# Optimization experiments

Measured on AMD Instinct MI355X. Metric: run time of the kernel, lower is better.

Reference implementation:

```python
import jax, jax.numpy as jnp
import numpy as np

EMBED_DIM = 768
NUM_HEADS = 12
HEAD_DIM = EMBED_DIM // NUM_HEADS


def setup_inputs() -> dict:
    key = jax.random.key(0)
    k1, k2, k3, k4, k5 = jax.random.split(key, 5)
    B, S, D = 2, 4096, EMBED_DIM
    scale = 1.0 / np.sqrt(D)
    return {
        "x": jax.random.normal(k1, (B, S, D), dtype=jnp.float32),
        "Wqkv": jax.random.normal(k2, (D, 3 * D), dtype=jnp.float32) * scale,
        "bqkv": jax.random.normal(k3, (3 * D,), dtype=jnp.float32) * 0.02,
        "Wout": jax.random.normal(k4, (D, D), dtype=jnp.float32) * scale,
        "bout": jax.random.normal(k5, (D,), dtype=jnp.float32) * 0.02,
    }


def reference(x, Wqkv, bqkv, Wout, bout):
    B, S, D = x.shape
    H, Hd = NUM_HEADS, HEAD_DIM
    # fused QKV projection: [B,S,3D]
    qkv = x @ Wqkv + bqkv
    q, k, v = jnp.split(qkv, 3, axis=-1)
    # [B,S,D] -> [B,H,S,Hd]
    q = q.reshape(B, S, H, Hd).transpose(0, 2, 1, 3)
    k = k.reshape(B, S, H, Hd).transpose(0, 2, 1, 3)
    v = v.reshape(B, S, H, Hd).transpose(0, 2, 1, 3)
    # causal SDPA (dropout_p = 0)
    scores = jnp.einsum("bhsd,bhtd->bhst", q, k) / jnp.sqrt(jnp.asarray(Hd, x.dtype))
    causal = jnp.tril(jnp.ones((S, S), dtype=bool))  # [S,S]
    scores = jnp.where(causal[None, None], scores, jnp.finfo(x.dtype).min)
    attn = jax.nn.softmax(scores, axis=-1)
    y = jnp.einsum("bhst,bhtd->bhsd", attn, v)  # [B,H,S,Hd]
    y = y.transpose(0, 2, 1, 3).reshape(B, S, D)
    return y @ Wout + bout
```

## Files before the change

### kernel.cpp

```cpp
#include <hip/hip_runtime.h>

#define S_LEN 4096
#define NH 12
#define HD 64
#define DMODEL 768
#define BATCH 2
#define MTOT (BATCH * S_LEN)

typedef __bf16 bf16x8 __attribute__((ext_vector_type(8)));
typedef __bf16 bf16x4 __attribute__((ext_vector_type(4)));
typedef float f32x4 __attribute__((ext_vector_type(4)));
typedef float f32x8 __attribute__((ext_vector_type(8)));

#define SM_SCALE_LOG2E 0.18033688f
#define SLAB_STRIDE 8448

__device__ __forceinline__ f32x4 f32x4_zero() {
  f32x4 z = {0.f, 0.f, 0.f, 0.f};
  return z;
}

__device__ __forceinline__ void async16(const __bf16* g, void* l) {
  __builtin_amdgcn_global_load_lds(
      (const __attribute__((address_space(1))) void*)g,
      (__attribute__((address_space(3))) void*)l, 16, 0, 0);
}

__global__ __launch_bounds__(256) void cvt_f32_bf16(const float* __restrict__ in,
                                                    __bf16* __restrict__ out, int n8) {
  int i = blockIdx.x * 256 + threadIdx.x;
  if (i >= n8) return;
  f32x8 a = ((const f32x8*)in)[i];
  bf16x8 o;
#pragma unroll
  for (int j = 0; j < 8; ++j) o[j] = (__bf16)a[j];
  ((bf16x8*)out)[i] = o;
}

__global__ __launch_bounds__(256) void transpose_cvt(const float* __restrict__ in,
                                                     __bf16* __restrict__ out, int N) {
  __shared__ __bf16 t[64][72];
  int kb = blockIdx.x * 64, nb = blockIdx.y * 64;
  int c = threadIdx.x & 63, r0 = threadIdx.x >> 6;
#pragma unroll
  for (int i = 0; i < 16; ++i) {
    int r = r0 * 16 + i;
    t[c][r] = (__bf16)in[(size_t)(kb + r) * N + nb + c];
  }
  __syncthreads();
#pragma unroll
  for (int i = 0; i < 16; ++i) {
    int r = r0 * 16 + i;
    out[(size_t)(nb + r) * DMODEL + kb + c] = t[r][c];
  }
}

__device__ __forceinline__ void gemm128_bt(const __bf16* __restrict__ A,
                                           const __bf16* __restrict__ Bt,
                                           int m0, int n0, int K,
                                           __bf16* Alds, __bf16* Blds,
                                           f32x4 acc[4][4]) {
  const int tid = threadIdx.x;
  const int l = tid & 63, w = tid >> 6;
  const int wr = w >> 1, wc = w & 1;
  const int g = l >> 4, ln = l & 15;

  const int rr = tid >> 3;
  const int sx = (tid & 7) ^ (rr & 7);
  const __bf16* As = A + (size_t)(m0 + rr) * K + sx * 8;
  const __bf16* Bs = Bt + (size_t)(n0 + rr) * K + sx * 8;
  char* Ad = (char*)Alds + (w << 10);
  char* Bd = (char*)Blds + (w << 10);

  for (int k0 = 0; k0 < K; k0 += 64) {
#pragma unroll
    for (int i = 0; i < 4; ++i) {
      async16(As + (size_t)(i * 32) * K + k0, Ad + i * 4096);
      async16(Bs + (size_t)(i * 32) * K + k0, Bd + i * 4096);
    }
    __syncthreads();
#pragma unroll
    for (int kk = 0; kk < 2; ++kk) {
      bf16x8 af[4], bfr[4];
#pragma unroll
      for (int mi = 0; mi < 4; ++mi) {
        int row = wr * 64 + mi * 16 + ln;
        af[mi] = *(const bf16x8*)(Alds + row * 64 + ((((kk << 2) + g) ^ (row & 7)) << 3));
      }
#pragma unroll
      for (int ni = 0; ni < 4; ++ni) {
        int row = wc * 64 + ni * 16 + ln;
        bfr[ni] = *(const bf16x8*)(Blds + row * 64 + ((((kk << 2) + g) ^ (row & 7)) << 3));
      }
#pragma unroll
      for (int mi = 0; mi < 4; ++mi)
#pragma unroll
        for (int ni = 0; ni < 4; ++ni)
          acc[mi][ni] =
              __builtin_amdgcn_mfma_f32_16x16x32_bf16(af[mi], bfr[ni], acc[mi][ni], 0, 0, 0);
    }
    __syncthreads();
  }
}

__global__ __launch_bounds__(256) void gemm_qkv(const __bf16* __restrict__ xb,
                                                const __bf16* __restrict__ Wt,
                                                const float* __restrict__ bqkv,
                                                __bf16* __restrict__ Qo,
                                                __bf16* __restrict__ Ko,
                                                __bf16* __restrict__ Vto) {
  __shared__ __bf16 Alds[128 * 64];
  __shared__ __bf16 Blds[128 * 64];
  int bm = blockIdx.x & 63, bn = blockIdx.x >> 6;
  int m0 = bm * 128, n0 = bn * 128;
  f32x4 acc[4][4];
#pragma unroll
  for (int i = 0; i < 4; ++i)
#pragma unroll
    for (int j = 0; j < 4; ++j) acc[i][j] = f32x4_zero();
  gemm128_bt(xb, Wt, m0, n0, DMODEL, Alds, Blds, acc);

  const int l = threadIdx.x & 63, w = threadIdx.x >> 6;
  const int wr = w >> 1, wc = w & 1, g = l >> 4, ln = l & 15;
#pragma unroll
  for (int ni = 0; ni < 4; ++ni) {
    int ncol = n0 + wc * 64 + ni * 16 + ln;
    int which = ncol / DMODEL;
    int dd = ncol - which * DMODEL;
    int h = dd >> 6, hd = dd & 63;
    float bias = bqkv[ncol];
    if (which == 2) {
#pragma unroll
      for (int mi = 0; mi < 4; ++mi)
#pragma unroll
        for (int r = 0; r < 4; ++r) {
          int mrow = m0 + wr * 64 + mi * 16 + 4 * g + r;
          int b = mrow >> 12, s = mrow & (S_LEN - 1);
          float v = acc[mi][ni][r] + bias;
          Vto[(((size_t)(b * NH + h) * HD) + hd) * S_LEN + s] = (__bf16)v;
        }
    } else {
      __bf16* op = (which == 0) ? Qo : Ko;
      const float scl = (which == 0) ? SM_SCALE_LOG2E : 1.0f;
#pragma unroll
      for (int mi = 0; mi < 4; ++mi)
#pragma unroll
        for (int r = 0; r < 4; ++r) {
          int mrow = m0 + wr * 64 + mi * 16 + 4 * g + r;
          int b = mrow >> 12, s = mrow & (S_LEN - 1);
          float v = (acc[mi][ni][r] + bias) * scl;
          op[((((size_t)b * NH + h) * S_LEN) + s) * HD + hd] = (__bf16)v;
        }
    }
  }
}

__global__ __launch_bounds__(256) void gemm_out(const __bf16* __restrict__ yb,
                                                const __bf16* __restrict__ Wt,
                                                const float* __restrict__ bout,
                                                float* __restrict__ out) {
  __shared__ __bf16 Alds[128 * 64];
  __shared__ __bf16 Blds[128 * 64];
  int bm = blockIdx.x & 63, bn = blockIdx.x >> 6;
  int m0 = bm * 128, n0 = bn * 128;
  f32x4 acc[4][4];
#pragma unroll
  for (int i = 0; i < 4; ++i)
#pragma unroll
    for (int j = 0; j < 4; ++j) acc[i][j] = f32x4_zero();
  gemm128_bt(yb, Wt, m0, n0, DMODEL, Alds, Blds, acc);

  const int l = threadIdx.x & 63, w = threadIdx.x >> 6;
  const int wr = w >> 1, wc = w & 1, g = l >> 4, ln = l & 15;
#pragma unroll
  for (int ni = 0; ni < 4; ++ni) {
    int ncol = n0 + wc * 64 + ni * 16 + ln;
    float bias = bout[ncol];
#pragma unroll
    for (int mi = 0; mi < 4; ++mi)
#pragma unroll
      for (int r = 0; r < 4; ++r) {
        int mrow = m0 + wr * 64 + mi * 16 + 4 * g + r;
        out[(size_t)mrow * DMODEL + ncol] = acc[mi][ni][r] + bias;
      }
  }
}

__global__ __launch_bounds__(256) void attn_fwd14(const __bf16* __restrict__ Q,
                                                  const __bf16* __restrict__ K,
                                                  const __bf16* __restrict__ Vt,
                                                  __bf16* __restrict__ Y,
                                                  char* __restrict__ Po) {
  __shared__ __bf16 KVl[2][2][4096];
  __shared__ char Plb[4][2048];

  const int tid = threadIdx.x;
  const int wv = tid >> 6, l = tid & 63;
  const int g = l >> 4, ln = l & 15;
  const int bi = blockIdx.x;
  const int xcd = bi & 7, j = bi >> 3;
  const int head = xcd * 3 + (j % 3);
  const int r_ = j / 3;

  int c, t0, t1, part;
  bool split;
  if (r_ < 64) {
    c = 63 - (r_ >> 1);
    part = r_ & 1;
    int T = c + 1;
    int h = (T + 1) >> 1;
    t0 = part ? h : 0;
    t1 = part ? T : h;
    split = true;
  } else {
    c = 95 - r_;
    part = 0;
    t0 = 0;
    t1 = c + 1;
    split = false;
  }
  const int q0 = 64 * c + 16 * wv;
  const int thr = 16 * wv + ln;
  const bool hasDiag = (t1 == c + 1);

  const size_t hb = (size_t)head * (S_LEN * HD);
  const __bf16* Qh = Q + hb;
  const __bf16* Kh = K + hb;
  const __bf16* Vh = Vt + hb;

  const int sw = (ln & 7) << 4;
  char* Pw = Plb[wv] + ln * 128;

  const int r0 = tid >> 3;
  const int s0 = (tid & 7) ^ (r0 & 7);
  const size_t kL0 = (size_t)r0 * HD + s0 * 8;
  const size_t kL1 = kL0 + (size_t)32 * HD;
  const size_t vL0 = (size_t)r0 * S_LEN + s0 * 8;
  const size_t vL1 = vL0 + (size_t)32 * S_LEN;
  const int ldsoff = wv << 10;

  bf16x8 qf[2];
#pragma unroll
  for (int t = 0; t < 2; ++t)
    qf[t] = *(const bf16x8*)(Qh + (size_t)(q0 + ln) * HD + 32 * t + 8 * g);

  bf16x8 ones;
#pragma unroll
  for (int t = 0; t < 8; ++t) ones[t] = (__bf16)1.0f;

  f32x4 o[4], o5;
#pragma unroll
  for (int nt = 0; nt < 4; ++nt) o[nt] = f32x4_zero();
  o5 = f32x4_zero();

  const __bf16* kq = Kh + (size_t)t0 * 64 * HD;
  const __bf16* vq = Vh + t0 * 64;
  {
    char* Kd = (char*)&KVl[0][0][0] + ldsoff;
    char* Vd = (char*)&KVl[0][1][0] + ldsoff;
    async16(kq + kL0, Kd);
    async16(kq + kL1, Kd + 4096);
    async16(vq + vL0, Vd);
    async16(vq + vL1, Vd + 4096);
    __syncthreads();
  }
  kq += (size_t)64 * HD;
  vq += 64;

  int cur = 0;
  for (int i = t0; i < t1; ++i) {
    const bool more = (i + 1) < t1;
    if (more) {
      char* Kd = (char*)&KVl[cur ^ 1][0][0] + ldsoff;
      char* Vd = (char*)&KVl[cur ^ 1][1][0] + ldsoff;
      async16(kq + kL0, Kd);
      async16(kq + kL1, Kd + 4096);
      async16(vq + vL0, Vd);
      async16(vq + vL1, Vd + 4096);
      kq += (size_t)64 * HD;
      vq += 64;
    }

    const __bf16* Kl = &KVl[cur][0][0];
    const __bf16* Vl = &KVl[cur][1][0];
    const bool diag = hasDiag && (i == c);

    if (!diag) {
#pragma unroll
      for (int jt = 0; jt < 4; ++jt) {
        int row = 16 * jt + ln;
        bf16x8 kf0 = *(const bf16x8*)(Kl + row * 64 + ((g ^ (row & 7)) << 3));
        bf16x8 kf1 = *(const bf16x8*)(Kl + row * 64 + (((4 + g) ^ (row & 7)) << 3));
        f32x4 z = f32x4_zero();
        z = __builtin_amdgcn_mfma_f32_16x16x32_bf16(kf0, qf[0], z, 0, 0, 0);
        z = __builtin_amdgcn_mfma_f32_16x16x32_bf16(kf1, qf[1], z, 0, 0, 0);
        bf16x4 qd;
#pragma unroll
        for (int r = 0; r < 4; ++r) qd[r] = (__bf16)__builtin_exp2f(z[r]);
        *(bf16x4*)(Pw + ((32 * jt + 8 * g) ^ sw)) = qd;
      }
    } else {
#pragma unroll
      for (int jt = 0; jt < 4; ++jt) {
        int row = 16 * jt + ln;
        bf16x8 kf0 = *(const bf16x8*)(Kl + row * 64 + ((g ^ (row & 7)) << 3));
        bf16x8 kf1 = *(const bf16x8*)(Kl + row * 64 + (((4 + g) ^ (row & 7)) << 3));
        f32x4 z = f32x4_zero();
        z = __builtin_amdgcn_mfma_f32_16x16x32_bf16(kf0, qf[0], z, 0, 0, 0);
        z = __builtin_amdgcn_mfma_f32_16x16x32_bf16(kf1, qf[1], z, 0, 0, 0);
        bf16x4 qd;
#pragma unroll
        for (int r = 0; r < 4; ++r) {
          float pv = __builtin_exp2f(z[r]);
          if (16 * jt + 4 * g + r > thr) pv = 0.f;
          qd[r] = (__bf16)pv;
        }
        *(bf16x4*)(Pw + ((32 * jt + 8 * g) ^ sw)) = qd;
      }
    }

    bf16x8 pa0 = *(const bf16x8*)(Pw + ((16 * g) ^ sw));
    bf16x8 pa1 = *(const bf16x8*)(Pw + ((64 + 16 * g) ^ sw));
    __builtin_amdgcn_s_setprio(1);
    o5 = __builtin_amdgcn_mfma_f32_16x16x32_bf16(pa0, ones, o5, 0, 0, 0);
    o5 = __builtin_amdgcn_mfma_f32_16x16x32_bf16(pa1, ones, o5, 0, 0, 0);
#pragma unroll
    for (int nt = 0; nt < 4; ++nt) {
      int row = 16 * nt + ln;
      bf16x8 vf0 = *(const bf16x8*)(Vl + row * 64 + ((g ^ (row & 7)) << 3));
      bf16x8 vf1 = *(const bf16x8*)(Vl + row * 64 + (((4 + g) ^ (row & 7)) << 3));
      o[nt] = __builtin_amdgcn_mfma_f32_16x16x32_bf16(pa0, vf0, o[nt], 0, 0, 0);
      o[nt] = __builtin_amdgcn_mfma_f32_16x16x32_bf16(pa1, vf1, o[nt], 0, 0, 0);
    }
    __builtin_amdgcn_s_setprio(0);

    if (more) __syncthreads();
    cur ^= 1;
  }

  if (!split) {
    const int bb = head / NH, hh = head - bb * NH;
    __bf16* Yp = Y + ((size_t)bb * S_LEN) * DMODEL + hh * HD;
#pragma unroll
    for (int r = 0; r < 4; ++r) {
      float inv = 1.0f / o5[r];
      int qr = q0 + 4 * g + r;
#pragma unroll
      for (int nt = 0; nt < 4; ++nt)
        Yp[(size_t)qr * DMODEL + 16 * nt + ln] = (__bf16)(o[nt][r] * inv);
    }
  } else {
    char* slab = Po + (size_t)(((head << 5) + (c - 32)) * 2 + part) * SLAB_STRIDE;
#pragma unroll
    for (int r = 0; r < 4; ++r) {
      int rowL = 16 * wv + 4 * g + r;
#pragma unroll
      for (int nt = 0; nt < 4; ++nt)
        *(__bf16*)(slab + (rowL * 64 + 16 * nt + ln) * 2) = (__bf16)o[nt][r];
      if (ln == 0) *(float*)(slab + 8192 + rowL * 4) = o5[r];
    }
  }
}

__global__ __launch_bounds__(256) void attn_combine(const char* __restrict__ Po,
                                                    __bf16* __restrict__ Y) {
  const int blk = blockIdx.x;
  const int head = blk >> 6, rem = blk & 63;
  const int cc = rem >> 1, half = rem & 1;
  const int c = cc + 32;
  const char* s0 = Po + (size_t)(((head << 5) + cc) * 2) * SLAB_STRIDE;
  const char* s1 = s0 + SLAB_STRIDE;
  const int tid = threadIdx.x;
  const int row = half * 32 + (tid >> 3), d0 = (tid & 7) * 8;

  bf16x8 a = *(const bf16x8*)(s0 + (row * 64 + d0) * 2);
  bf16x8 b = *(const bf16x8*)(s1 + (row * 64 + d0) * 2);
  float rs = *(const float*)(s0 + 8192 + row * 4) + *(const float*)(s1 + 8192 + row * 4);
  float inv = 1.0f / rs;

  const int bb = head / NH, hh = head - bb * NH;
  __bf16* yp = Y + ((size_t)bb * S_LEN + 64 * c + row) * DMODEL + hh * HD + d0;
  bf16x8 o;
#pragma unroll
  for (int j = 0; j < 8; ++j) o[j] = (__bf16)(((float)a[j] + (float)b[j]) * inv);
  *(bf16x8*)yp = o;
}

extern "C" void kernel_launch(void* const* d_in, const int* in_sizes, int n_in,
                              void* d_out, int out_size, void* d_ws, size_t ws_size,
                              hipStream_t stream) {
  const float* x = (const float*)d_in[0];
  const float* Wqkv = (const float*)d_in[1];
  const float* bqkv = (const float*)d_in[2];
  const float* Wout = (const float*)d_in[3];
  const float* bout = (const float*)d_in[4];
  float* out = (float*)d_out;

  char* ws = (char*)d_ws;
  size_t off = 0;
  auto take = [&](size_t bytes) {
    char* p = ws + off;
    off += bytes;
    return p;
  };
  const size_t MD2 = (size_t)MTOT * DMODEL * 2;
  __bf16* xb = (__bf16*)take(MD2);
  __bf16* Wqkv_t = (__bf16*)take((size_t)3 * DMODEL * DMODEL * 2);
  __bf16* Wout_t = (__bf16*)take((size_t)DMODEL * DMODEL * 2);
  __bf16* Qb = (__bf16*)take(MD2);
  __bf16* Kb = (__bf16*)take(MD2);
  __bf16* Vtb = (__bf16*)take(MD2);
  __bf16* Yb = (__bf16*)take(MD2);
  char* Po = take((size_t)1536 * SLAB_STRIDE);

  int n8 = MTOT * DMODEL / 8;
  cvt_f32_bf16<<<(n8 + 255) / 256, 256, 0, stream>>>(x, xb, n8);
  transpose_cvt<<<dim3(DMODEL / 64, 3 * DMODEL / 64), 256, 0, stream>>>(Wqkv, Wqkv_t, 3 * DMODEL);
  transpose_cvt<<<dim3(DMODEL / 64, DMODEL / 64), 256, 0, stream>>>(Wout, Wout_t, DMODEL);
  gemm_qkv<<<64 * (3 * DMODEL / 128), 256, 0, stream>>>(xb, Wqkv_t, bqkv, Qb, Kb, Vtb);
  attn_fwd14<<<2304, 256, 0, stream>>>(Qb, Kb, Vtb, Yb, Po);
  attn_combine<<<1536, 256, 0, stream>>>(Po, Yb);
  gemm_out<<<64 * (DMODEL / 128), 256, 0, stream>>>(Yb, Wout_t, bout, out);
}
```

Before: 183.2 us.

## Process two 64-row query tiles per attention block to share K/V loads

The attention kernel now gives each block 128 query rows, split into two 64-row subtiles (A and B). Both subtiles are computed from the same double-buffered K/V tiles in shared memory, which halves K/V global traffic and the number of barriers per query row. The work split, slab layout and combine indexing are rescaled to match, and the launch drops to half as many blocks. In exchange each block holds more registers (two sets of accumulators and Q fragments), and coarser blocks may balance the causal workload less evenly.

New measurement: 212.9 us. +16.2%, slower.

```diff
diff --git a/kernel.cpp b/kernel.cpp
--- a/kernel.cpp
+++ b/kernel.cpp
@@ -13,7 +13,7 @@
 typedef float f32x8 __attribute__((ext_vector_type(8)));
 
 #define SM_SCALE_LOG2E 0.18033688f
-#define SLAB_STRIDE 8448
+#define SLAB_STRIDE 16896
 
 __device__ __forceinline__ f32x4 f32x4_zero() {
   f32x4 z = {0.f, 0.f, 0.f, 0.f};
@@ -186,7 +186,7 @@
   }
 }
 
-__global__ __launch_bounds__(256) void attn_fwd14(const __bf16* __restrict__ Q,
+__global__ __launch_bounds__(256) void attn_fwd16(const __bf16* __restrict__ Q,
                                                   const __bf16* __restrict__ K,
                                                   const __bf16* __restrict__ Vt,
                                                   __bf16* __restrict__ Y,
@@ -204,24 +204,24 @@
 
   int c, t0, t1, part;
   bool split;
-  if (r_ < 64) {
-    c = 63 - (r_ >> 1);
+  if (r_ < 32) {
+    c = 31 - (r_ >> 1);
     part = r_ & 1;
-    int T = c + 1;
-    int h = (T + 1) >> 1;
+    int h = c + 1;
     t0 = part ? h : 0;
-    t1 = part ? T : h;
+    t1 = part ? 2 * c + 2 : h;
     split = true;
   } else {
-    c = 95 - r_;
+    c = 47 - r_;
     part = 0;
     t0 = 0;
-    t1 = c + 1;
+    t1 = 2 * c + 2;
     split = false;
   }
-  const int q0 = 64 * c + 16 * wv;
+  const int q0A = 128 * c + 16 * wv;
+  const int q0B = q0A + 64;
   const int thr = 16 * wv + ln;
-  const bool hasDiag = (t1 == c + 1);
+  const int iA = 2 * c, iB = 2 * c + 1;
 
   const size_t hb = (size_t)head * (S_LEN * HD);
   const __bf16* Qh = Q + hb;
@@ -239,19 +239,25 @@
   const size_t vL1 = vL0 + (size_t)32 * S_LEN;
   const int ldsoff = wv << 10;
 
-  bf16x8 qf[2];
-#pragma unroll
-  for (int t = 0; t < 2; ++t)
-    qf[t] = *(const bf16x8*)(Qh + (size_t)(q0 + ln) * HD + 32 * t + 8 * g);
+  bf16x8 qfA[2], qfB[2];
+#pragma unroll
+  for (int t = 0; t < 2; ++t) {
+    qfA[t] = *(const bf16x8*)(Qh + (size_t)(q0A + ln) * HD + 32 * t + 8 * g);
+    qfB[t] = *(const bf16x8*)(Qh + (size_t)(q0B + ln) * HD + 32 * t + 8 * g);
+  }
 
   bf16x8 ones;
 #pragma unroll
   for (int t = 0; t < 8; ++t) ones[t] = (__bf16)1.0f;
 
-  f32x4 o[4], o5;
-#pragma unroll
-  for (int nt = 0; nt < 4; ++nt) o[nt] = f32x4_zero();
-  o5 = f32x4_zero();
+  f32x4 oA[4], oB[4], o5A, o5B;
+#pragma unroll
+  for (int nt = 0; nt < 4; ++nt) {
+    oA[nt] = f32x4_zero();
+    oB[nt] = f32x4_zero();
+  }
+  o5A = f32x4_zero();
+  o5B = f32x4_zero();
 
   const __bf16* kq = Kh + (size_t)t0 * 64 * HD;
   const __bf16* vq = Vh + t0 * 64;
@@ -283,56 +289,108 @@
 
     const __bf16* Kl = &KVl[cur][0][0];
     const __bf16* Vl = &KVl[cur][1][0];
-    const bool diag = hasDiag && (i == c);
-
-    if (!diag) {
-#pragma unroll
-      for (int jt = 0; jt < 4; ++jt) {
-        int row = 16 * jt + ln;
-        bf16x8 kf0 = *(const bf16x8*)(Kl + row * 64 + ((g ^ (row & 7)) << 3));
-        bf16x8 kf1 = *(const bf16x8*)(Kl + row * 64 + (((4 + g) ^ (row & 7)) << 3));
-        f32x4 z = f32x4_zero();
-        z = __builtin_amdgcn_mfma_f32_16x16x32_bf16(kf0, qf[0], z, 0, 0, 0);
-        z = __builtin_amdgcn_mfma_f32_16x16x32_bf16(kf1, qf[1], z, 0, 0, 0);
-        bf16x4 qd;
-#pragma unroll
-        for (int r = 0; r < 4; ++r) qd[r] = (__bf16)__builtin_exp2f(z[r]);
-        *(bf16x4*)(Pw + ((32 * jt + 8 * g) ^ sw)) = qd;
-      }
-    } else {
-#pragma unroll
-      for (int jt = 0; jt < 4; ++jt) {
-        int row = 16 * jt + ln;
-        bf16x8 kf0 = *(const bf16x8*)(Kl + row * 64 + ((g ^ (row & 7)) << 3));
-        bf16x8 kf1 = *(const bf16x8*)(Kl + row * 64 + (((4 + g) ^ (row & 7)) << 3));
-        f32x4 z = f32x4_zero();
-        z = __builtin_amdgcn_mfma_f32_16x16x32_bf16(kf0, qf[0], z, 0, 0, 0);
-        z = __builtin_amdgcn_mfma_f32_16x16x32_bf16(kf1, qf[1], z, 0, 0, 0);
-        bf16x4 qd;
-#pragma unroll
-        for (int r = 0; r < 4; ++r) {
-          float pv = __builtin_exp2f(z[r]);
-          if (16 * jt + 4 * g + r > thr) pv = 0.f;
-          qd[r] = (__bf16)pv;
-        }
-        *(bf16x4*)(Pw + ((32 * jt + 8 * g) ^ sw)) = qd;
-      }
-    }
-
-    bf16x8 pa0 = *(const bf16x8*)(Pw + ((16 * g) ^ sw));
-    bf16x8 pa1 = *(const bf16x8*)(Pw + ((64 + 16 * g) ^ sw));
-    __builtin_amdgcn_s_setprio(1);
-    o5 = __builtin_amdgcn_mfma_f32_16x16x32_bf16(pa0, ones, o5, 0, 0, 0);
-    o5 = __builtin_amdgcn_mfma_f32_16x16x32_bf16(pa1, ones, o5, 0, 0, 0);
-#pragma unroll
-    for (int nt = 0; nt < 4; ++nt) {
-      int row = 16 * nt + ln;
-      bf16x8 vf0 = *(const bf16x8*)(Vl + row * 64 + ((g ^ (row & 7)) << 3));
-      bf16x8 vf1 = *(const bf16x8*)(Vl + row * 64 + (((4 + g) ^ (row & 7)) << 3));
-      o[nt] = __builtin_amdgcn_mfma_f32_16x16x32_bf16(pa0, vf0, o[nt], 0, 0, 0);
-      o[nt] = __builtin_amdgcn_mfma_f32_16x16x32_bf16(pa1, vf1, o[nt], 0, 0, 0);
-    }
-    __builtin_amdgcn_s_setprio(0);
+
+    if (i <= iA) {
+      const bool diag = (i == iA);
+      if (!diag) {
+#pragma unroll
+        for (int jt = 0; jt < 4; ++jt) {
+          int row = 16 * jt + ln;
+          bf16x8 kf0 = *(const bf16x8*)(Kl + row * 64 + ((g ^ (row & 7)) << 3));
+          bf16x8 kf1 = *(const bf16x8*)(Kl + row * 64 + (((4 + g) ^ (row & 7)) << 3));
+          f32x4 z = f32x4_zero();
+          z = __builtin_amdgcn_mfma_f32_16x16x32_bf16(kf0, qfA[0], z, 0, 0, 0);
+          z = __builtin_amdgcn_mfma_f32_16x16x32_bf16(kf1, qfA[1], z, 0, 0, 0);
+          bf16x4 qd;
+#pragma unroll
+          for (int r = 0; r < 4; ++r) qd[r] = (__bf16)__builtin_exp2f(z[r]);
+          *(bf16x4*)(Pw + ((32 * jt + 8 * g) ^ sw)) = qd;
+        }
+      } else {
+#pragma unroll
+        for (int jt = 0; jt < 4; ++jt) {
+          int row = 16 * jt + ln;
+          bf16x8 kf0 = *(const bf16x8*)(Kl + row * 64 + ((g ^ (row & 7)) << 3));
+          bf16x8 kf1 = *(const bf16x8*)(Kl + row * 64 + (((4 + g) ^ (row & 7)) << 3));
+          f32x4 z = f32x4_zero();
+          z = __builtin_amdgcn_mfma_f32_16x16x32_bf16(kf0, qfA[0], z, 0, 0, 0);
+          z = __builtin_amdgcn_mfma_f32_16x16x32_bf16(kf1, qfA[1], z, 0, 0, 0);
+          bf16x4 qd;
+#pragma unroll
+          for (int r = 0; r < 4; ++r) {
+            float pv = __builtin_exp2f(z[r]);
+            if (16 * jt + 4 * g + r > thr) pv = 0.f;
+            qd[r] = (__bf16)pv;
+          }
+          *(bf16x4*)(Pw + ((32 * jt + 8 * g) ^ sw)) = qd;
+        }
+      }
+      bf16x8 pa0 = *(const bf16x8*)(Pw + ((16 * g) ^ sw));
+      bf16x8 pa1 = *(const bf16x8*)(Pw + ((64 + 16 * g) ^ sw));
+      __builtin_amdgcn_s_setprio(1);
+      o5A = __builtin_amdgcn_mfma_f32_16x16x32_bf16(pa0, ones, o5A, 0, 0, 0);
+      o5A = __builtin_amdgcn_mfma_f32_16x16x32_bf16(pa1, ones, o5A, 0, 0, 0);
+#pragma unroll
+      for (int nt = 0; nt < 4; ++nt) {
+        int row = 16 * nt + ln;
+        bf16x8 vf0 = *(const bf16x8*)(Vl + row * 64 + ((g ^ (row & 7)) << 3));
+        bf16x8 vf1 = *(const bf16x8*)(Vl + row * 64 + (((4 + g) ^ (row & 7)) << 3));
+        oA[nt] = __builtin_amdgcn_mfma_f32_16x16x32_bf16(pa0, vf0, oA[nt], 0, 0, 0);
+        oA[nt] = __builtin_amdgcn_mfma_f32_16x16x32_bf16(pa1, vf1, oA[nt], 0, 0, 0);
+      }
+      __builtin_amdgcn_s_setprio(0);
+    }
+
+    {
+      const bool diag = (i == iB);
+      if (!diag) {
+#pragma unroll
+        for (int jt = 0; jt < 4; ++jt) {
+          int row = 16 * jt + ln;
+          bf16x8 kf0 = *(const bf16x8*)(Kl + row * 64 + ((g ^ (row & 7)) << 3));
+          bf16x8 kf1 = *(const bf16x8*)(Kl + row * 64 + (((4 + g) ^ (row & 7)) << 3));
+          f32x4 z = f32x4_zero();
+          z = __builtin_amdgcn_mfma_f32_16x16x32_bf16(kf0, qfB[0], z, 0, 0, 0);
+          z = __builtin_amdgcn_mfma_f32_16x16x32_bf16(kf1, qfB[1], z, 0, 0, 0);
+          bf16x4 qd;
+#pragma unroll
+          for (int r = 0; r < 4; ++r) qd[r] = (__bf16)__builtin_exp2f(z[r]);
+          *(bf16x4*)(Pw + ((32 * jt + 8 * g) ^ sw)) = qd;
+        }
+      } else {
+#pragma unroll
+        for (int jt = 0; jt < 4; ++jt) {
+          int row = 16 * jt + ln;
+          bf16x8 kf0 = *(const bf16x8*)(Kl + row * 64 + ((g ^ (row & 7)) << 3));
+          bf16x8 kf1 = *(const bf16x8*)(Kl + row * 64 + (((4 + g) ^ (row & 7)) << 3));
+          f32x4 z = f32x4_zero();
+          z = __builtin_amdgcn_mfma_f32_16x16x32_bf16(kf0, qfB[0], z, 0, 0, 0);
+          z = __builtin_amdgcn_mfma_f32_16x16x32_bf16(kf1, qfB[1], z, 0, 0, 0);
+          bf16x4 qd;
+#pragma unroll
+          for (int r = 0; r < 4; ++r) {
+            float pv = __builtin_exp2f(z[r]);
+            if (16 * jt + 4 * g + r > thr) pv = 0.f;
+            qd[r] = (__bf16)pv;
+          }
+          *(bf16x4*)(Pw + ((32 * jt + 8 * g) ^ sw)) = qd;
+        }
+      }
+      bf16x8 pa0 = *(const bf16x8*)(Pw + ((16 * g) ^ sw));
+      bf16x8 pa1 = *(const bf16x8*)(Pw + ((64 + 16 * g) ^ sw));
+      __builtin_amdgcn_s_setprio(1);
+      o5B = __builtin_amdgcn_mfma_f32_16x16x32_bf16(pa0, ones, o5B, 0, 0, 0);
+      o5B = __builtin_amdgcn_mfma_f32_16x16x32_bf16(pa1, ones, o5B, 0, 0, 0);
+#pragma unroll
+      for (int nt = 0; nt < 4; ++nt) {
+        int row = 16 * nt + ln;
+        bf16x8 vf0 = *(const bf16x8*)(Vl + row * 64 + ((g ^ (row & 7)) << 3));
+        bf16x8 vf1 = *(const bf16x8*)(Vl + row * 64 + (((4 + g) ^ (row & 7)) << 3));
+        oB[nt] = __builtin_amdgcn_mfma_f32_16x16x32_bf16(pa0, vf0, oB[nt], 0, 0, 0);
+        oB[nt] = __builtin_amdgcn_mfma_f32_16x16x32_bf16(pa1, vf1, oB[nt], 0, 0, 0);
+      }
+      __builtin_amdgcn_s_setprio(0);
+    }
 
     if (more) __syncthreads();
     cur ^= 1;
@@ -343,21 +401,29 @@
     __bf16* Yp = Y + ((size_t)bb * S_LEN) * DMODEL + hh * HD;
 #pragma unroll
     for (int r = 0; r < 4; ++r) {
-      float inv = 1.0f / o5[r];
-      int qr = q0 + 4 * g + r;
-#pragma unroll
-      for (int nt = 0; nt < 4; ++nt)
-        Yp[(size_t)qr * DMODEL + 16 * nt + ln] = (__bf16)(o[nt][r] * inv);
+      float invA = 1.0f / o5A[r];
+      float invB = 1.0f / o5B[r];
+      int qrA = q0A + 4 * g + r, qrB = q0B + 4 * g + r;
+#pragma unroll
+      for (int nt = 0; nt < 4; ++nt) {
+        Yp[(size_t)qrA * DMODEL + 16 * nt + ln] = (__bf16)(oA[nt][r] * invA);
+        Yp[(size_t)qrB * DMODEL + 16 * nt + ln] = (__bf16)(oB[nt][r] * invB);
+      }
     }
   } else {
-    char* slab = Po + (size_t)(((head << 5) + (c - 32)) * 2 + part) * SLAB_STRIDE;
+    char* slab = Po + (size_t)(((head << 4) + (c - 16)) * 2 + part) * SLAB_STRIDE;
 #pragma unroll
     for (int r = 0; r < 4; ++r) {
-      int rowL = 16 * wv + 4 * g + r;
-#pragma unroll
-      for (int nt = 0; nt < 4; ++nt)
-        *(__bf16*)(slab + (rowL * 64 + 16 * nt + ln) * 2) = (__bf16)o[nt][r];
-      if (ln == 0) *(float*)(slab + 8192 + rowL * 4) = o5[r];
+      int rowA = 16 * wv + 4 * g + r, rowB = 64 + rowA;
+#pragma unroll
+      for (int nt = 0; nt < 4; ++nt) {
+        *(__bf16*)(slab + (rowA * 64 + 16 * nt + ln) * 2) = (__bf16)oA[nt][r];
+        *(__bf16*)(slab + (rowB * 64 + 16 * nt + ln) * 2) = (__bf16)oB[nt][r];
+      }
+      if (ln == 0) {
+        *(float*)(slab + 16384 + rowA * 4) = o5A[r];
+        *(float*)(slab + 16384 + rowB * 4) = o5B[r];
+      }
     }
   }
 }
@@ -366,20 +432,20 @@
                                                     __bf16* __restrict__ Y) {
   const int blk = blockIdx.x;
   const int head = blk >> 6, rem = blk & 63;
-  const int cc = rem >> 1, half = rem & 1;
-  const int c = cc + 32;
-  const char* s0 = Po + (size_t)(((head << 5) + cc) * 2) * SLAB_STRIDE;
+  const int cc = rem >> 2, quarter = rem & 3;
+  const int c = cc + 16;
+  const char* s0 = Po + (size_t)(((head << 4) + cc) * 2) * SLAB_STRIDE;
   const char* s1 = s0 + SLAB_STRIDE;
   const int tid = threadIdx.x;
-  const int row = half * 32 + (tid >> 3), d0 = (tid & 7) * 8;
+  const int row = quarter * 32 + (tid >> 3), d0 = (tid & 7) * 8;
 
   bf16x8 a = *(const bf16x8*)(s0 + (row * 64 + d0) * 2);
   bf16x8 b = *(const bf16x8*)(s1 + (row * 64 + d0) * 2);
-  float rs = *(const float*)(s0 + 8192 + row * 4) + *(const float*)(s1 + 8192 + row * 4);
+  float rs = *(const float*)(s0 + 16384 + row * 4) + *(const float*)(s1 + 16384 + row * 4);
   float inv = 1.0f / rs;
 
   const int bb = head / NH, hh = head - bb * NH;
-  __bf16* yp = Y + ((size_t)bb * S_LEN + 64 * c + row) * DMODEL + hh * HD + d0;
+  __bf16* yp = Y + ((size_t)bb * S_LEN + 128 * c + row) * DMODEL + hh * HD + d0;
   bf16x8 o;
 #pragma unroll
   for (int j = 0; j < 8; ++j) o[j] = (__bf16)(((float)a[j] + (float)b[j]) * inv);
@@ -411,14 +477,14 @@
   __bf16* Kb = (__bf16*)take(MD2);
   __bf16* Vtb = (__bf16*)take(MD2);
   __bf16* Yb = (__bf16*)take(MD2);
-  char* Po = take((size_t)1536 * SLAB_STRIDE);
+  char* Po = take((size_t)768 * SLAB_STRIDE);
 
   int n8 = MTOT * DMODEL / 8;
   cvt_f32_bf16<<<(n8 + 255) / 256, 256, 0, stream>>>(x, xb, n8);
   transpose_cvt<<<dim3(DMODEL / 64, 3 * DMODEL / 64), 256, 0, stream>>>(Wqkv, Wqkv_t, 3 * DMODEL);
   transpose_cvt<<<dim3(DMODEL / 64, DMODEL / 64), 256, 0, stream>>>(Wout, Wout_t, DMODEL);
   gemm_qkv<<<64 * (3 * DMODEL / 128), 256, 0, stream>>>(xb, Wqkv_t, bqkv, Qb, Kb, Vtb);
-  attn_fwd14<<<2304, 256, 0, stream>>>(Qb, Kb, Vtb, Yb, Po);
+  attn_fwd16<<<1152, 256, 0, stream>>>(Qb, Kb, Vtb, Yb, Po);
   attn_combine<<<1536, 256, 0, stream>>>(Po, Yb);
   gemm_out<<<64 * (DMODEL / 128), 256, 0, stream>>>(Yb, Wout_t, bout, out);
 }
```

## Split causal attention KV range into up to four parts by query-block length

Applied to the files above, without the earlier changes.

Replaces the two-way KV split for the longest query blocks with a graded split: the longest 16 query blocks per head get four parts, the next 16 get three, the next 16 get two, and the shortest stay unsplit. Work per block becomes more uniform and the grid grows from 2304 to 3840 blocks, reducing the long tail of the causal attention kernel. The combine kernel now sums a variable number of partial slabs for more rows, adding more partial-output traffic and combine work.

Measured after the change: 179.1 us. -2.3%, faster.

```diff
diff --git a/kernel.cpp b/kernel.cpp
--- a/kernel.cpp
+++ b/kernel.cpp
@@ -186,7 +186,7 @@
   }
 }
 
-__global__ __launch_bounds__(256) void attn_fwd14(const __bf16* __restrict__ Q,
+__global__ __launch_bounds__(256) void attn_fwd17(const __bf16* __restrict__ Q,
                                                   const __bf16* __restrict__ K,
                                                   const __bf16* __restrict__ Vt,
                                                   __bf16* __restrict__ Y,
@@ -202,26 +202,39 @@
   const int head = xcd * 3 + (j % 3);
   const int r_ = j / 3;
 
-  int c, t0, t1, part;
+  int c, part, np;
   bool split;
   if (r_ < 64) {
-    c = 63 - (r_ >> 1);
-    part = r_ & 1;
-    int T = c + 1;
-    int h = (T + 1) >> 1;
-    t0 = part ? h : 0;
-    t1 = part ? T : h;
+    c = 63 - (r_ >> 2);
+    part = r_ & 3;
+    np = 4;
+    split = true;
+  } else if (r_ < 112) {
+    int q = r_ - 64;
+    c = 47 - q / 3;
+    part = q % 3;
+    np = 3;
+    split = true;
+  } else if (r_ < 144) {
+    int q = r_ - 112;
+    c = 31 - (q >> 1);
+    part = q & 1;
+    np = 2;
     split = true;
   } else {
-    c = 95 - r_;
+    c = 159 - r_;
     part = 0;
-    t0 = 0;
-    t1 = c + 1;
+    np = 1;
     split = false;
   }
+  const int T = c + 1;
+  const int base = T / np, rem = T % np;
+  const int t0 = part * base + (part < rem ? part : rem);
+  const int t1 = t0 + base + (part < rem ? 1 : 0);
+
   const int q0 = 64 * c + 16 * wv;
   const int thr = 16 * wv + ln;
-  const bool hasDiag = (t1 == c + 1);
+  const bool hasDiag = (t1 == T);
 
   const size_t hb = (size_t)head * (S_LEN * HD);
   const __bf16* Qh = Q + hb;
@@ -350,7 +363,11 @@
         Yp[(size_t)qr * DMODEL + 16 * nt + ln] = (__bf16)(o[nt][r] * inv);
     }
   } else {
-    char* slab = Po + (size_t)(((head << 5) + (c - 32)) * 2 + part) * SLAB_STRIDE;
+    int soff;
+    if (c < 32) soff = (c - 16) * 2 + part;
+    else if (c < 48) soff = 32 + (c - 32) * 3 + part;
+    else soff = 80 + (c - 48) * 4 + part;
+    char* slab = Po + ((size_t)head * 144 + soff) * SLAB_STRIDE;
 #pragma unroll
     for (int r = 0; r < 4; ++r) {
       int rowL = 16 * wv + 4 * g + r;
@@ -365,24 +382,39 @@
 __global__ __launch_bounds__(256) void attn_combine(const char* __restrict__ Po,
                                                     __bf16* __restrict__ Y) {
   const int blk = blockIdx.x;
-  const int head = blk >> 6, rem = blk & 63;
+  const int head = blk / 96, rem = blk - head * 96;
   const int cc = rem >> 1, half = rem & 1;
-  const int c = cc + 32;
-  const char* s0 = Po + (size_t)(((head << 5) + cc) * 2) * SLAB_STRIDE;
-  const char* s1 = s0 + SLAB_STRIDE;
+  const int c = cc + 16;
+  int np, boff;
+  if (c < 32) {
+    np = 2;
+    boff = (c - 16) * 2;
+  } else if (c < 48) {
+    np = 3;
+    boff = 32 + (c - 32) * 3;
+  } else {
+    np = 4;
+    boff = 80 + (c - 48) * 4;
+  }
+  const char* s = Po + ((size_t)head * 144 + boff) * SLAB_STRIDE;
   const int tid = threadIdx.x;
   const int row = half * 32 + (tid >> 3), d0 = (tid & 7) * 8;
 
-  bf16x8 a = *(const bf16x8*)(s0 + (row * 64 + d0) * 2);
-  bf16x8 b = *(const bf16x8*)(s1 + (row * 64 + d0) * 2);
-  float rs = *(const float*)(s0 + 8192 + row * 4) + *(const float*)(s1 + 8192 + row * 4);
+  float acc[8] = {0.f, 0.f, 0.f, 0.f, 0.f, 0.f, 0.f, 0.f};
+  float rs = 0.f;
+  for (int p = 0; p < np; ++p) {
+    bf16x8 a = *(const bf16x8*)(s + (size_t)p * SLAB_STRIDE + (row * 64 + d0) * 2);
+#pragma unroll
+    for (int j = 0; j < 8; ++j) acc[j] += (float)a[j];
+    rs += *(const float*)(s + (size_t)p * SLAB_STRIDE + 8192 + row * 4);
+  }
   float inv = 1.0f / rs;
 
   const int bb = head / NH, hh = head - bb * NH;
   __bf16* yp = Y + ((size_t)bb * S_LEN + 64 * c + row) * DMODEL + hh * HD + d0;
   bf16x8 o;
 #pragma unroll
-  for (int j = 0; j < 8; ++j) o[j] = (__bf16)(((float)a[j] + (float)b[j]) * inv);
+  for (int j = 0; j < 8; ++j) o[j] = (__bf16)(acc[j] * inv);
   *(bf16x8*)yp = o;
 }
 
@@ -411,14 +443,14 @@
   __bf16* Kb = (__bf16*)take(MD2);
   __bf16* Vtb = (__bf16*)take(MD2);
   __bf16* Yb = (__bf16*)take(MD2);
-  char* Po = take((size_t)1536 * SLAB_STRIDE);
+  char* Po = take((size_t)24 * 144 * SLAB_STRIDE);
 
   int n8 = MTOT * DMODEL / 8;
   cvt_f32_bf16<<<(n8 + 255) / 256, 256, 0, stream>>>(x, xb, n8);
   transpose_cvt<<<dim3(DMODEL / 64, 3 * DMODEL / 64), 256, 0, stream>>>(Wqkv, Wqkv_t, 3 * DMODEL);
   transpose_cvt<<<dim3(DMODEL / 64, DMODEL / 64), 256, 0, stream>>>(Wout, Wout_t, DMODEL);
   gemm_qkv<<<64 * (3 * DMODEL / 128), 256, 0, stream>>>(xb, Wqkv_t, bqkv, Qb, Kb, Vtb);
-  attn_fwd14<<<2304, 256, 0, stream>>>(Qb, Kb, Vtb, Yb, Po);
-  attn_combine<<<1536, 256, 0, stream>>>(Po, Yb);
+  attn_fwd17<<<3840, 256, 0, stream>>>(Qb, Kb, Vtb, Yb, Po);
+  attn_combine<<<2304, 256, 0, stream>>>(Po, Yb);
   gemm_out<<<64 * (DMODEL / 128), 256, 0, stream>>>(Yb, Wout_t, bout, out);
 }
```
